# Kernel optimization log

Measured on AMD Instinct MI355X. Metric: run time of the kernel, lower is better.

Reference implementation:

```python
import jax, jax.numpy as jnp
import numpy as np

N = 100000  # nodes
E = 1600000  # directed edges

_DIMS = [("eg1", 3, 160), ("eg2", 160, 80), ("eg3", 80, 40), ("eg4", 40, 20),
         ("el1", 20, 10), ("el2", 10, 3), ("dl1", 3, 10), ("dl2", 10, 20),
         ("dg1", 20, 40), ("dg2", 40, 80), ("dg3", 80, 160), ("dg4", 160, 3)]


def _lin_init(key, ci, co):
    s = 1.0 / np.sqrt(ci)
    kw, kb = jax.random.split(key)
    w = jax.random.uniform(kw, (ci, co), jnp.float32, -s, s)
    b = jax.random.uniform(kb, (co,), jnp.float32, -s, s)
    return w, b


def setup_inputs():
    key = jax.random.key(0)
    k0, k1, k2 = jax.random.split(key, 3)
    x = jax.random.normal(k0, (N, 3), jnp.float32)
    src = jax.random.randint(k1, (E,), 0, N)
    dst = jax.random.randint(k2, (E,), 0, N)
    edge_index = jnp.stack([src, dst])  # [2, E] int32 indices
    out = {"x": x, "edge_index": edge_index}
    for i, (name, ci, co) in enumerate(_DIMS):
        w, b = _lin_init(jax.random.fold_in(key, i + 10), ci, co)
        out[name + "_w"] = w
        out[name + "_b"] = b
    return out


def _gcn(x, w, b, src, dst, norm):
    # PyG GCNConv: linear transform, then symmetric-normalized scatter-add.
    h = x @ w
    agg = jax.ops.segment_sum(h[src] * norm[:, None], dst, num_segments=N)
    return agg + b


def reference(x, edge_index, eg1_w, eg1_b, eg2_w, eg2_b, eg3_w, eg3_b, eg4_w, eg4_b,
              el1_w, el1_b, el2_w, el2_b, dl1_w, dl1_b, dl2_w, dl2_b,
              dg1_w, dg1_b, dg2_w, dg2_b, dg3_w, dg3_b, dg4_w, dg4_b):
    loops = jnp.arange(N)
    src = jnp.concatenate([edge_index[0], loops])  # add self-loops (PyG default)
    dst = jnp.concatenate([edge_index[1], loops])
    deg = jax.ops.segment_sum(jnp.ones(src.shape[0], x.dtype), dst, num_segments=N)
    dis = jnp.where(deg > 0, jax.lax.rsqrt(deg), 0.0)
    norm = dis[src] * dis[dst]  # D^-1/2 A D^-1/2 edge weights
    relu = jax.nn.relu
    h = relu(_gcn(x, eg1_w, eg1_b, src, dst, norm))
    h = relu(_gcn(h, eg2_w, eg2_b, src, dst, norm))
    h = relu(_gcn(h, eg3_w, eg3_b, src, dst, norm))
    h = relu(_gcn(h, eg4_w, eg4_b, src, dst, norm))
    h = relu(h @ el1_w + el1_b)
    h = h @ el2_w + el2_b  # latent [N, 3]
    h = relu(h @ dl1_w + dl1_b)
    h = relu(h @ dl2_w + dl2_b)
    h = relu(_gcn(h, dg1_w, dg1_b, src, dst, norm))
    h = relu(_gcn(h, dg2_w, dg2_b, src, dst, norm))
    h = relu(_gcn(h, dg3_w, dg3_b, src, dst, norm))
    h = jnp.tanh(_gcn(h, dg4_w, dg4_b, src, dst, norm))
    return h
```

## Files before the change

kernel.cpp:

```cpp
#include <hip/hip_runtime.h>
#include <hip/hip_fp16.h>
#include <math.h>

#define BS 256
static constexpr int NN = 100000;
static constexpr int EE = 1600000;
static constexpr int BUCKET_SH = 7;
static constexpr int NBUCKET = (NN + 127) >> BUCKET_SH;
static constexpr int NB_PART = 256;
static constexpr int CHUNK = EE / NB_PART;
static constexpr int NP_ = NBUCKET * NB_PART;
static constexpr int SCAN_ELEMS = 1024;
static constexpr int NPB = (NP_ + SCAN_ELEMS - 1) / SCAN_ELEMS;

static inline int cdiv(long long a, int b) { return (int)((a + b - 1) / b); }

typedef _Float16 half8 __attribute__((ext_vector_type(8)));
typedef float f32x4 __attribute__((ext_vector_type(4)));

template <int ACT>
__device__ __forceinline__ float act_f(float v) {
    if (ACT == 1) return fmaxf(v, 0.0f);
    if (ACT == 2) return tanhf(v);
    return v;
}

__device__ __forceinline__ unsigned short h16(float v) {
    return __half_as_ushort(__float2half(v));
}
__device__ __forceinline__ unsigned pack2h(float a, float b) {
    return (unsigned)h16(a) | ((unsigned)h16(b) << 16);
}
__device__ __forceinline__ float4 cvt4h(uint2 r) {
    float2 fa = __half22float2(*(const __half2*)&r.x);
    float2 fb = __half22float2(*(const __half2*)&r.y);
    return make_float4(fa.x, fa.y, fb.x, fb.y);
}
__device__ __forceinline__ void acc8h(uint4 r, float4& a, float4& b) {
    float2 f0 = __half22float2(*(const __half2*)&r.x);
    float2 f1 = __half22float2(*(const __half2*)&r.y);
    float2 f2 = __half22float2(*(const __half2*)&r.z);
    float2 f3 = __half22float2(*(const __half2*)&r.w);
    a.x += f0.x; a.y += f0.y; a.z += f1.x; a.w += f1.y;
    b.x += f2.x; b.y += f2.y; b.z += f3.x; b.w += f3.y;
}

template <int OUTM>
__device__ __forceinline__ void store1(float* out, size_t idx, float v, float dn) {
    if (OUTM == 0) out[idx] = v;
    else if (OUTM == 1) out[idx] = v * dn;
    else if (OUTM == 2) ((unsigned short*)out)[idx] = h16(v * dn);
    else ((unsigned short*)out)[idx] = h16(v);
}

__global__ __launch_bounds__(256) void k_hist(const int* __restrict__ dst,
                                              int* __restrict__ part_cnt) {
    __shared__ int h[NBUCKET];
    int b = blockIdx.x;
    for (int j = threadIdx.x; j < NBUCKET; j += 256) h[j] = 0;
    __syncthreads();
    int e0 = b * CHUNK;
    for (int k = threadIdx.x; k < CHUNK; k += 256)
        atomicAdd(&h[dst[e0 + k] >> BUCKET_SH], 1);
    __syncthreads();
    for (int j = threadIdx.x; j < NBUCKET; j += 256)
        part_cnt[j * NB_PART + b] = h[j];
}

__global__ void k_scanA(const int* __restrict__ in, int* __restrict__ outp,
                        int* __restrict__ bsums) {
    __shared__ int lds[BS];
    int base = blockIdx.x * SCAN_ELEMS;
    int t = threadIdx.x;
    int v[4];
    int s = 0;
#pragma unroll
    for (int j = 0; j < 4; ++j) {
        int idx = base + t * 4 + j;
        v[j] = (idx < NP_) ? in[idx] : 0;
        s += v[j];
    }
    lds[t] = s;
    __syncthreads();
    for (int off = 1; off < BS; off <<= 1) {
        int add = (t >= off) ? lds[t - off] : 0;
        __syncthreads();
        lds[t] += add;
        __syncthreads();
    }
    int run = lds[t] - s;
    if (t == BS - 1) bsums[blockIdx.x] = lds[BS - 1];
#pragma unroll
    for (int j = 0; j < 4; ++j) {
        int idx = base + t * 4 + j;
        if (idx < NP_) outp[idx] = run;
        run += v[j];
    }
}

__global__ void k_scanB(int* __restrict__ bsums) {
    if (threadIdx.x == 0 && blockIdx.x == 0) {
        int acc = 0;
        for (int i = 0; i < NPB; ++i) {
            int t = bsums[i];
            bsums[i] = acc;
            acc += t;
        }
    }
}

__global__ void k_scanC(int* __restrict__ outp, const int* __restrict__ bsums,
                        int* __restrict__ bbase) {
    int i = blockIdx.x * BS + threadIdx.x;
    if (i < NP_) {
        int v = outp[i] + bsums[i / SCAN_ELEMS];
        outp[i] = v;
        if ((i & (NB_PART - 1)) == 0) bbase[i / NB_PART] = v;
    }
    if (i == 0) bbase[NBUCKET] = EE;
}

__global__ __launch_bounds__(256) void k_part(const int* __restrict__ src,
                                              const int* __restrict__ dst,
                                              const int* __restrict__ scan_out,
                                              unsigned* __restrict__ epb) {
    __shared__ int cur[NBUCKET];
    int b = blockIdx.x;
    for (int j = threadIdx.x; j < NBUCKET; j += 256) cur[j] = scan_out[j * NB_PART + b];
    __syncthreads();
    int e0 = b * CHUNK;
    for (int k = threadIdx.x; k < CHUNK; k += 256) {
        int e = e0 + k;
        int d = dst[e];
        int s = src[e];
        int pos = atomicAdd(&cur[d >> BUCKET_SH], 1);
        epb[pos] = ((unsigned)(d & ((1 << BUCKET_SH) - 1)) << 17) | (unsigned)s;
    }
}

__global__ __launch_bounds__(256) void k_fine2(const int* __restrict__ bbase,
                                               const unsigned* __restrict__ epb,
                                               int* __restrict__ eidx,
                                               int* __restrict__ rowptr,
                                               float* __restrict__ dis) {
    __shared__ int hcnt[1 << BUCKET_SH];
    __shared__ int hoff[1 << BUCKET_SH];
    int b = blockIdx.x;
    int n0 = b << BUCKET_SH;
    int nloc = min(1 << BUCKET_SH, NN - n0);
    int t = threadIdx.x;
    if (t < (1 << BUCKET_SH)) hcnt[t] = 0;
    __syncthreads();
    int es = bbase[b], ee = bbase[b + 1];
    for (int k = es + t; k < ee; k += 256) atomicAdd(&hcnt[epb[k] >> 17], 1);
    __syncthreads();
    if (t < (1 << BUCKET_SH)) hoff[t] = hcnt[t];
    __syncthreads();
    for (int off = 1; off < (1 << BUCKET_SH); off <<= 1) {
        int add = (t >= off && t < (1 << BUCKET_SH)) ? hoff[t - off] : 0;
        __syncthreads();
        if (t < (1 << BUCKET_SH)) hoff[t] += add;
        __syncthreads();
    }
    if (t < nloc) {
        int excl = hoff[t] - hcnt[t];
        rowptr[n0 + t] = es + excl;
        dis[n0 + t] = rsqrtf((float)(hcnt[t] + 1));
    }
    __syncthreads();
    if (t < (1 << BUCKET_SH)) hoff[t] = es + hoff[t] - hcnt[t];
    __syncthreads();
    for (int k = es + t; k < ee; k += 256) {
        unsigned p = epb[k];
        int pos = atomicAdd(&hoff[p >> 17], 1);
        eidx[pos] = (int)(p & 0x1FFFFu);
    }
    if (b == NBUCKET - 1 && t == 0) rowptr[NN] = EE;
}

template <int C, int ACT, bool HASB, bool OUTH>
__global__ void k_gatherw(const unsigned short* __restrict__ g, const int* __restrict__ rowptr,
                          const int* __restrict__ eidx, const float* __restrict__ dis,
                          const float* __restrict__ b, float* __restrict__ out) {
    static_assert(C % 8 == 0, "C%8");
    constexpr int V = C / 8;
    int t = blockIdx.x * BS + threadIdx.x;
    if (t >= NN * V) return;
    int n = t / V, v = t % V;
    const uint4* g4 = (const uint4*)g;
    float4 accA = make_float4(0.f, 0.f, 0.f, 0.f);
    float4 accB = make_float4(0.f, 0.f, 0.f, 0.f);
    acc8h(g4[(size_t)n * V + v], accA, accB);
    int rs = rowptr[n], re = rowptr[n + 1];
    int k = rs;
    for (; k + 4 <= re; k += 4) {
        int s0 = eidx[k + 0], s1 = eidx[k + 1], s2 = eidx[k + 2], s3 = eidx[k + 3];
        uint4 r0 = g4[(size_t)s0 * V + v];
        uint4 r1 = g4[(size_t)s1 * V + v];
        uint4 r2 = g4[(size_t)s2 * V + v];
        uint4 r3 = g4[(size_t)s3 * V + v];
        acc8h(r0, accA, accB);
        acc8h(r1, accA, accB);
        acc8h(r2, accA, accB);
        acc8h(r3, accA, accB);
    }
    for (; k < re; ++k) {
        acc8h(g4[(size_t)eidx[k] * V + v], accA, accB);
    }
    float dn = dis[n];
    accA.x *= dn; accA.y *= dn; accA.z *= dn; accA.w *= dn;
    accB.x *= dn; accB.y *= dn; accB.z *= dn; accB.w *= dn;
    if (HASB) {
        float4 b0 = ((const float4*)b)[v * 2 + 0];
        float4 b1 = ((const float4*)b)[v * 2 + 1];
        accA.x += b0.x; accA.y += b0.y; accA.z += b0.z; accA.w += b0.w;
        accB.x += b1.x; accB.y += b1.y; accB.z += b1.z; accB.w += b1.w;
    }
    accA.x = act_f<ACT>(accA.x); accA.y = act_f<ACT>(accA.y);
    accA.z = act_f<ACT>(accA.z); accA.w = act_f<ACT>(accA.w);
    accB.x = act_f<ACT>(accB.x); accB.y = act_f<ACT>(accB.y);
    accB.z = act_f<ACT>(accB.z); accB.w = act_f<ACT>(accB.w);
    if (OUTH) {
        uint4 u;
        u.x = pack2h(accA.x, accA.y);
        u.y = pack2h(accA.z, accA.w);
        u.z = pack2h(accB.x, accB.y);
        u.w = pack2h(accB.z, accB.w);
        ((uint4*)out)[(size_t)n * V + v] = u;
    } else {
        float4* op = (float4*)out + (size_t)n * (C / 4) + v * 2;
        op[0] = accA;
        op[1] = accB;
    }
}

template <int C, int ACT, bool HASB, bool OUTH>
__global__ void k_gatherh(const unsigned short* __restrict__ g, const int* __restrict__ rowptr,
                          const int* __restrict__ eidx, const float* __restrict__ dis,
                          const float* __restrict__ b, float* __restrict__ out) {
    static_assert(C % 4 == 0, "C%4");
    constexpr int V = C / 4;
    int t = blockIdx.x * BS + threadIdx.x;
    if (t >= NN * V) return;
    int n = t / V, v = t % V;
    const uint2* g2 = (const uint2*)g;
    float4 acc = cvt4h(g2[(size_t)n * V + v]);
    int rs = rowptr[n], re = rowptr[n + 1];
    int k = rs;
    for (; k + 4 <= re; k += 4) {
        int s0 = eidx[k + 0], s1 = eidx[k + 1], s2 = eidx[k + 2], s3 = eidx[k + 3];
        uint2 r0 = g2[(size_t)s0 * V + v];
        uint2 r1 = g2[(size_t)s1 * V + v];
        uint2 r2 = g2[(size_t)s2 * V + v];
        uint2 r3 = g2[(size_t)s3 * V + v];
        float4 h0 = cvt4h(r0), h1 = cvt4h(r1), h2 = cvt4h(r2), h3 = cvt4h(r3);
        acc.x += (h0.x + h1.x) + (h2.x + h3.x);
        acc.y += (h0.y + h1.y) + (h2.y + h3.y);
        acc.z += (h0.z + h1.z) + (h2.z + h3.z);
        acc.w += (h0.w + h1.w) + (h2.w + h3.w);
    }
    for (; k < re; ++k) {
        float4 hv = cvt4h(g2[(size_t)eidx[k] * V + v]);
        acc.x += hv.x; acc.y += hv.y; acc.z += hv.z; acc.w += hv.w;
    }
    float dn = dis[n];
    acc.x *= dn; acc.y *= dn; acc.z *= dn; acc.w *= dn;
    if (HASB) {
        float4 bb = ((const float4*)b)[v];
        acc.x += bb.x; acc.y += bb.y; acc.z += bb.z; acc.w += bb.w;
    }
    acc.x = act_f<ACT>(acc.x);
    acc.y = act_f<ACT>(acc.y);
    acc.z = act_f<ACT>(acc.z);
    acc.w = act_f<ACT>(acc.w);
    if (OUTH) {
        uint2 u;
        u.x = pack2h(acc.x, acc.y);
        u.y = pack2h(acc.z, acc.w);
        ((uint2*)out)[(size_t)n * V + v] = u;
    } else {
        ((float4*)out)[(size_t)n * V + v] = acc;
    }
}

template <int ACT, bool HASB>
__global__ void k_gather3d(const float* __restrict__ g, const int* __restrict__ rowptr,
                           const int* __restrict__ eidx, const float* __restrict__ dis,
                           const float* __restrict__ b, float* __restrict__ out) {
    int n = blockIdx.x * BS + threadIdx.x;
    if (n >= NN) return;
    const float* gp = g + (size_t)n * 3;
    float a0 = gp[0], a1 = gp[1], a2 = gp[2];
    int rs = rowptr[n], re = rowptr[n + 1];
    int k = rs;
    for (; k + 4 <= re; k += 4) {
        const float* q0 = g + (size_t)eidx[k + 0] * 3;
        const float* q1 = g + (size_t)eidx[k + 1] * 3;
        const float* q2 = g + (size_t)eidx[k + 2] * 3;
        const float* q3 = g + (size_t)eidx[k + 3] * 3;
        float b00 = q0[0], b01 = q0[1], b02 = q0[2];
        float b10 = q1[0], b11 = q1[1], b12 = q1[2];
        float b20 = q2[0], b21 = q2[1], b22 = q2[2];
        float b30 = q3[0], b31 = q3[1], b32 = q3[2];
        a0 += (b00 + b10) + (b20 + b30);
        a1 += (b01 + b11) + (b21 + b31);
        a2 += (b02 + b12) + (b22 + b32);
    }
    for (; k < re; ++k) {
        const float* gq = g + (size_t)eidx[k] * 3;
        a0 += gq[0]; a1 += gq[1]; a2 += gq[2];
    }
    float dn = dis[n];
    a0 *= dn; a1 *= dn; a2 *= dn;
    if (HASB) { a0 += b[0]; a1 += b[1]; a2 += b[2]; }
    float* op = out + (size_t)n * 3;
    op[0] = act_f<ACT>(a0);
    op[1] = act_f<ACT>(a1);
    op[2] = act_f<ACT>(a2);
}

__global__ void k_scale3(const float* __restrict__ x, const float* __restrict__ dis,
                         float* __restrict__ g) {
    int i = blockIdx.x * BS + threadIdx.x;
    if (i < NN * 3) g[i] = x[i] * dis[i / 3];
}

__global__ __launch_bounds__(256) void k_latent(const unsigned short* __restrict__ in20,
                                                const float* __restrict__ el1_w, const float* __restrict__ el1_b,
                                                const float* __restrict__ el2_w, const float* __restrict__ el2_b,
                                                const float* __restrict__ dl1_w, const float* __restrict__ dl1_b,
                                                const float* __restrict__ dl2_w, const float* __restrict__ dl2_b,
                                                const float* __restrict__ dis,
                                                unsigned short* __restrict__ G) {
    __shared__ float w1[200], b1[10], w2[30], b2[3], w3[30], b3[10], w4[200], b4[20];
    int t = threadIdx.x;
    if (t < 200) w1[t] = el1_w[t];
    if (t < 10) b1[t] = el1_b[t];
    if (t < 30) w2[t] = el2_w[t];
    if (t < 3) b2[t] = el2_b[t];
    if (t < 30) w3[t] = dl1_w[t];
    if (t < 10) b3[t] = dl1_b[t];
    if (t < 200) w4[t] = dl2_w[t];
    if (t < 20) b4[t] = dl2_b[t];
    __syncthreads();
    int n = blockIdx.x * 256 + t;
    if (n >= NN) return;
    float h0[20];
    const uint2* ip = (const uint2*)in20 + (size_t)n * 5;
#pragma unroll
    for (int v = 0; v < 5; ++v) {
        float4 f = cvt4h(ip[v]);
        h0[v * 4 + 0] = f.x; h0[v * 4 + 1] = f.y;
        h0[v * 4 + 2] = f.z; h0[v * 4 + 3] = f.w;
    }
    float a1[10];
#pragma unroll
    for (int j = 0; j < 10; ++j) {
        float s = b1[j];
#pragma unroll
        for (int i = 0; i < 20; ++i) s = fmaf(h0[i], w1[i * 10 + j], s);
        a1[j] = fmaxf(s, 0.0f);
    }
    float a2[3];
#pragma unroll
    for (int j = 0; j < 3; ++j) {
        float s = b2[j];
#pragma unroll
        for (int i = 0; i < 10; ++i) s = fmaf(a1[i], w2[i * 3 + j], s);
        a2[j] = s;
    }
    float a3[10];
#pragma unroll
    for (int j = 0; j < 10; ++j) {
        float s = b3[j];
#pragma unroll
        for (int i = 0; i < 3; ++i) s = fmaf(a2[i], w3[i * 10 + j], s);
        a3[j] = fmaxf(s, 0.0f);
    }
    float dn = dis[n];
    uint2* gp = (uint2*)G + (size_t)n * 5;
#pragma unroll
    for (int v = 0; v < 5; ++v) {
        float o[4];
#pragma unroll
        for (int q = 0; q < 4; ++q) {
            int j = v * 4 + q;
            float s = b4[j];
#pragma unroll
            for (int i = 0; i < 10; ++i) s = fmaf(a3[i], w4[i * 20 + j], s);
            o[q] = fmaxf(s, 0.0f) * dn;
        }
        uint2 u;
        u.x = pack2h(o[0], o[1]);
        u.y = pack2h(o[2], o[3]);
        gp[v] = u;
    }
}

template <int K, int N, int ACT, bool HASB, int OUTM>
__global__ __launch_bounds__(256) void k_mm_mfma(const unsigned short* __restrict__ x,
                                                 const float* __restrict__ w,
                                                 const float* __restrict__ bias,
                                                 unsigned short* __restrict__ out,
                                                 const float* __restrict__ dis) {
    constexpr int KP = (K + 31) & ~31;
    constexpr int NT = (N + 15) / 16;
    constexpr int NPAD = NT * 16;
    constexpr int KC = KP / 32;
    constexpr int SP = KP + 8;
    __shared__ _Float16 Al[64 * SP];
    __shared__ _Float16 Wl[(KP / 8) * NPAD * 8];
    const int tid = threadIdx.x;
    const int n0 = blockIdx.x * 64;

    {
        constexpr int K4 = KP / 4;
        const uint2* x2 = (const uint2*)x;
        for (int i = tid; i < 64 * K4; i += 256) {
            int r = i / K4, k4 = i % K4;
            uint2 v = make_uint2(0u, 0u);
            int row = n0 + r;
            if (row < NN && k4 * 4 < K) v = x2[(size_t)row * (K / 4) + k4];
            *(uint2*)&Al[r * SP + k4 * 4] = v;
        }
    }
    for (int i = tid; i < KP * NPAD; i += 256) {
        int k = i / NPAD, n = i % NPAD;
        float v = (k < K && n < N) ? w[k * N + n] : 0.0f;
        Wl[(k >> 3) * NPAD * 8 + n * 8 + (k & 7)] = (_Float16)v;
    }
    __syncthreads();

    const int wave = tid >> 6;
    const int lane = tid & 63;
    const int lm = lane & 15;
    const int quad = lane >> 4;

    f32x4 acc[NT];
#pragma unroll
    for (int t = 0; t < NT; ++t) acc[t] = (f32x4){0.f, 0.f, 0.f, 0.f};

    const int arow = wave * 16 + lm;
#pragma unroll
    for (int kc = 0; kc < KC; ++kc) {
        half8 a = *(const half8*)&Al[arow * SP + kc * 32 + quad * 8];
#pragma unroll
        for (int t = 0; t < NT; ++t) {
            half8 bf = *(const half8*)&Wl[(kc * 4 + quad) * NPAD * 8 + (t * 16 + lm) * 8];
            acc[t] = __builtin_amdgcn_mfma_f32_16x16x32_f16(a, bf, acc[t], 0, 0, 0);
        }
    }
#pragma unroll
    for (int t = 0; t < NT; ++t) {
        int col = t * 16 + lm;
        if (col < N) {
            float bb = HASB ? bias[col] : 0.0f;
#pragma unroll
            for (int r = 0; r < 4; ++r) {
                int row = n0 + wave * 16 + quad * 4 + r;
                if (row < NN) {
                    float v = act_f<ACT>(acc[t][r] + bb);
                    if (OUTM == 2) v *= dis[row];
                    out[(size_t)row * N + col] = h16(v);
                }
            }
        }
    }
}

template <int CIN, int COUT, int ACT, int OUTM>
__global__ void k_mm_rowbcast(const float* __restrict__ x, const float* __restrict__ w,
                              const float* __restrict__ b, float* __restrict__ out) {
    static_assert(COUT % 4 == 0, "c4");
    constexpr int COUT4 = COUT / 4;
    int i = blockIdx.x * BS + threadIdx.x;
    if (i >= NN * COUT4) return;
    int n = i / COUT4, c4 = i % COUT4;
    const float4* w4 = (const float4*)w;
    float4 acc = ((const float4*)b)[c4];
    const float* xr = x + (size_t)n * CIN;
#pragma unroll
    for (int ci = 0; ci < CIN; ++ci) {
        float xv = xr[ci];
        float4 wv = w4[ci * COUT4 + c4];
        acc.x = fmaf(xv, wv.x, acc.x);
        acc.y = fmaf(xv, wv.y, acc.y);
        acc.z = fmaf(xv, wv.z, acc.z);
        acc.w = fmaf(xv, wv.w, acc.w);
    }
    acc.x = act_f<ACT>(acc.x); acc.y = act_f<ACT>(acc.y);
    acc.z = act_f<ACT>(acc.z); acc.w = act_f<ACT>(acc.w);
    if (OUTM == 3) {
        uint2 u;
        u.x = pack2h(acc.x, acc.y);
        u.y = pack2h(acc.z, acc.w);
        ((uint2*)out)[(size_t)n * COUT4 + c4] = u;
    } else {
        ((float4*)out)[(size_t)n * COUT4 + c4] = acc;
    }
}

template <int CIN, int COUT, int ACT, bool HASB, int OUTM, bool INH>
__global__ void k_mm_vec4(const float* __restrict__ x, const float* __restrict__ w,
                          const float* __restrict__ b, float* __restrict__ out,
                          const float* __restrict__ dis) {
    static_assert(CIN % 4 == 0 && COUT % 4 == 0, "align");
    constexpr int TM = 8;
    constexpr int CIN4 = CIN / 4;
    constexpr int COUT4 = COUT / 4;
    constexpr int RG = NN / TM;
    int i = blockIdx.x * BS + threadIdx.x;
    if (i >= RG * COUT4) return;
    int c4 = i % COUT4;
    int n0 = (i / COUT4) * TM;
    const float4* x4 = (const float4*)x;
    const uint2* xh = (const uint2*)x;
    const float4* w4 = (const float4*)w;
    float4 acc[TM];
    float4 bb = HASB ? ((const float4*)b)[c4] : make_float4(0.f, 0.f, 0.f, 0.f);
#pragma unroll
    for (int r = 0; r < TM; ++r) acc[r] = bb;
    for (int k4 = 0; k4 < CIN4; ++k4) {
        float4 wv[4];
#pragma unroll
        for (int j = 0; j < 4; ++j) wv[j] = w4[(size_t)(4 * k4 + j) * COUT4 + c4];
#pragma unroll
        for (int r = 0; r < TM; ++r) {
            float4 xv;
            if (INH) xv = cvt4h(xh[(size_t)(n0 + r) * CIN4 + k4]);
            else xv = x4[(size_t)(n0 + r) * CIN4 + k4];
            acc[r].x = fmaf(xv.x, wv[0].x, fmaf(xv.y, wv[1].x, fmaf(xv.z, wv[2].x, fmaf(xv.w, wv[3].x, acc[r].x))));
            acc[r].y = fmaf(xv.x, wv[0].y, fmaf(xv.y, wv[1].y, fmaf(xv.z, wv[2].y, fmaf(xv.w, wv[3].y, acc[r].y))));
            acc[r].z = fmaf(xv.x, wv[0].z, fmaf(xv.y, wv[1].z, fmaf(xv.z, wv[2].z, fmaf(xv.w, wv[3].z, acc[r].z))));
            acc[r].w = fmaf(xv.x, wv[0].w, fmaf(xv.y, wv[1].w, fmaf(xv.z, wv[2].w, fmaf(xv.w, wv[3].w, acc[r].w))));
        }
    }
#pragma unroll
    for (int r = 0; r < TM; ++r) {
        float vx = act_f<ACT>(acc[r].x), vy = act_f<ACT>(acc[r].y);
        float vz = act_f<ACT>(acc[r].z), vw = act_f<ACT>(acc[r].w);
        size_t gi = (size_t)(n0 + r) * COUT4 + c4;
        if (OUTM == 2) {
            float dn = dis[n0 + r];
            uint2 u;
            u.x = pack2h(vx * dn, vy * dn);
            u.y = pack2h(vz * dn, vw * dn);
            ((uint2*)out)[gi] = u;
        } else if (OUTM == 1) {
            float dn = dis[n0 + r];
            ((float4*)out)[gi] = make_float4(vx * dn, vy * dn, vz * dn, vw * dn);
        } else {
            ((float4*)out)[gi] = make_float4(vx, vy, vz, vw);
        }
    }
}

template <int CIN, int COUT, int ACT, bool HASB, int OUTM, bool INH>
__global__ void k_mm_vec(const float* __restrict__ x, const float* __restrict__ w,
                         const float* __restrict__ b, float* __restrict__ out,
                         const float* __restrict__ dis) {
    static_assert(CIN % 4 == 0, "CIN%4");
    constexpr int TM = 8;
    constexpr int CIN4 = CIN / 4;
    constexpr int RG = NN / TM;
    int i = blockIdx.x * BS + threadIdx.x;
    if (i >= RG * COUT) return;
    int c = i % COUT;
    int n0 = (i / COUT) * TM;
    float acc[TM];
    float bb = HASB ? b[c] : 0.0f;
#pragma unroll
    for (int r = 0; r < TM; ++r) acc[r] = bb;
    const float4* x4 = (const float4*)x;
    const uint2* xh = (const uint2*)x;
    for (int k = 0; k < CIN4; ++k) {
        float w0 = w[(4 * k + 0) * COUT + c];
        float w1 = w[(4 * k + 1) * COUT + c];
        float w2 = w[(4 * k + 2) * COUT + c];
        float w3 = w[(4 * k + 3) * COUT + c];
#pragma unroll
        for (int r = 0; r < TM; ++r) {
            float4 xv;
            if (INH) xv = cvt4h(xh[(size_t)(n0 + r) * CIN4 + k]);
            else xv = x4[(size_t)(n0 + r) * CIN4 + k];
            acc[r] = fmaf(xv.x, w0, fmaf(xv.y, w1, fmaf(xv.z, w2, fmaf(xv.w, w3, acc[r]))));
        }
    }
#pragma unroll
    for (int r = 0; r < TM; ++r) {
        int row = n0 + r;
        float dn = (OUTM == 1 || OUTM == 2) ? dis[row] : 0.0f;
        store1<OUTM>(out, (size_t)row * COUT + c, act_f<ACT>(acc[r]), dn);
    }
}

extern "C" void kernel_launch(void* const* d_in, const int* in_sizes, int n_in,
                              void* d_out, int out_size, void* d_ws, size_t ws_size,
                              hipStream_t stream) {
    const float* x = (const float*)d_in[0];
    const int* ei = (const int*)d_in[1];
    const int* src = ei;
    const int* dst = ei + EE;
    const float* eg1_w = (const float*)d_in[2];  const float* eg1_b = (const float*)d_in[3];
    const float* eg2_w = (const float*)d_in[4];  const float* eg2_b = (const float*)d_in[5];
    const float* eg3_w = (const float*)d_in[6];  const float* eg3_b = (const float*)d_in[7];
    const float* eg4_w = (const float*)d_in[8];  const float* eg4_b = (const float*)d_in[9];
    const float* el1_w = (const float*)d_in[10]; const float* el1_b = (const float*)d_in[11];
    const float* el2_w = (const float*)d_in[12]; const float* el2_b = (const float*)d_in[13];
    const float* dl1_w = (const float*)d_in[14]; const float* dl1_b = (const float*)d_in[15];
    const float* dl2_w = (const float*)d_in[16]; const float* dl2_b = (const float*)d_in[17];
    const float* dg1_w = (const float*)d_in[18]; const float* dg1_b = (const float*)d_in[19];
    const float* dg2_w = (const float*)d_in[20]; const float* dg2_b = (const float*)d_in[21];
    const float* dg3_w = (const float*)d_in[22]; const float* dg3_b = (const float*)d_in[23];
    const float* dg4_w = (const float*)d_in[24]; const float* dg4_b = (const float*)d_in[25];
    float* out = (float*)d_out;

    char* ws = (char*)d_ws;
    size_t off = 0;
    auto alloc = [&](size_t bytes) {
        void* p = ws + off;
        off += (bytes + 15) & ~(size_t)15;
        return p;
    };
    int* part_cnt = (int*)alloc(sizeof(int) * NP_);
    int* scan_out = (int*)alloc(sizeof(int) * NP_);
    int* bsums    = (int*)alloc(sizeof(int) * NPB);
    int* bbase    = (int*)alloc(sizeof(int) * (NBUCKET + 1));
    int* rowptr   = (int*)alloc(sizeof(int) * (NN + 1));
    float* dis    = (float*)alloc(sizeof(float) * NN);
    int* eidx     = (int*)alloc(sizeof(int) * EE);
    unsigned* epb = (unsigned*)alloc(sizeof(unsigned) * EE);
    unsigned short* G = (unsigned short*)alloc(sizeof(unsigned short) * 80 * (size_t)NN);
    float* bufA = (float*)alloc(sizeof(float) * 160 * (size_t)NN);
    float* bufB = (float*)alloc(sizeof(float) * 160 * (size_t)NN);

    k_hist<<<NB_PART, 256, 0, stream>>>(dst, part_cnt);
    k_scanA<<<NPB, BS, 0, stream>>>(part_cnt, scan_out, bsums);
    k_scanB<<<1, 64, 0, stream>>>(bsums);
    k_scanC<<<cdiv(NP_, BS), BS, 0, stream>>>(scan_out, bsums, bbase);
    k_part<<<NB_PART, 256, 0, stream>>>(src, dst, scan_out, epb);
    k_fine2<<<NBUCKET, 256, 0, stream>>>(bbase, epb, eidx, rowptr, dis);

    k_scale3<<<cdiv(3LL * NN, BS), BS, 0, stream>>>(x, dis, bufB);
    k_gather3d<0, false><<<cdiv(NN, BS), BS, 0, stream>>>(bufB, rowptr, eidx, dis, nullptr, bufA);
    k_mm_rowbcast<3, 160, 1, 3><<<cdiv(NN * 40LL, BS), BS, 0, stream>>>(bufA, eg1_w, eg1_b, bufB);

    k_mm_mfma<160, 80, 0, false, 2><<<cdiv(NN, 64), 256, 0, stream>>>(
        (const unsigned short*)bufB, eg2_w, nullptr, G, dis);
    k_gatherw<80, 1, true, true><<<cdiv(NN * 10LL, BS), BS, 0, stream>>>(G, rowptr, eidx, dis, eg2_b, bufA);

    k_mm_mfma<80, 40, 0, false, 2><<<cdiv(NN, 64), 256, 0, stream>>>(
        (const unsigned short*)bufA, eg3_w, nullptr, G, dis);
    k_gatherw<40, 1, true, true><<<cdiv(NN * 5LL, BS), BS, 0, stream>>>(G, rowptr, eidx, dis, eg3_b, bufB);

    k_mm_vec4<40, 20, 0, false, 2, true><<<cdiv((NN / 8) * 5LL, BS), BS, 0, stream>>>(
        bufB, eg4_w, nullptr, (float*)G, dis);
    k_gatherh<20, 1, true, true><<<cdiv(NN * 5LL, BS), BS, 0, stream>>>(G, rowptr, eidx, dis, eg4_b, bufA);

    k_latent<<<cdiv(NN, 256), 256, 0, stream>>>((const unsigned short*)bufA,
        el1_w, el1_b, el2_w, el2_b, dl1_w, dl1_b, dl2_w, dl2_b, dis, G);

    k_gatherh<20, 0, false, true><<<cdiv(NN * 5LL, BS), BS, 0, stream>>>(G, rowptr, eidx, dis, nullptr, bufA);
    k_mm_vec4<20, 40, 1, true, 2, true><<<cdiv((NN / 8) * 10LL, BS), BS, 0, stream>>>(
        bufA, dg1_w, dg1_b, (float*)G, dis);

    k_gatherw<40, 0, false, true><<<cdiv(NN * 5LL, BS), BS, 0, stream>>>(G, rowptr, eidx, dis, nullptr, bufB);
    k_mm_mfma<40, 80, 1, true, 2><<<cdiv(NN, 64), 256, 0, stream>>>(
        (const unsigned short*)bufB, dg2_w, dg2_b, G, dis);

    k_gatherw<80, 0, false, true><<<cdiv(NN * 10LL, BS), BS, 0, stream>>>(G, rowptr, eidx, dis, nullptr, bufA);
    k_mm_mfma<80, 160, 1, true, 3><<<cdiv(NN, 64), 256, 0, stream>>>(
        (const unsigned short*)bufA, dg3_w, dg3_b, (unsigned short*)bufB, nullptr);

    k_mm_vec<160, 3, 0, false, 1, true><<<cdiv((NN / 8) * 3LL, BS), BS, 0, stream>>>(bufB, dg4_w, nullptr, bufA, dis);
    k_gather3d<2, true><<<cdiv(NN, BS), BS, 0, stream>>>(bufA, rowptr, eidx, dis, dg4_b, out);
}
```

Before: 593.3 us.

## Pre-pack fp16 MFMA weights once and load operands directly from global

Adds a small per-layer kernel that converts each MFMA layer's fp32 weights into the padded fp16 fragment layout once per call. The MFMA matmul now reads A rows and weight fragments straight from global memory instead of staging them in LDS, which removes the per-block weight conversion, the LDS fill and the __syncthreads. The epilogue is reordered to loop over rows, hoisting the bias and dis loads. The trade-off is four extra tiny launches and uncached-looking global loads of B fragments that rely on L1/L2 reuse across blocks.

```diff
diff --git a/kernel.cpp b/kernel.cpp
--- a/kernel.cpp
+++ b/kernel.cpp
@@ -397,71 +397,70 @@
     }
 }
 
-template <int K, int N, int ACT, bool HASB, int OUTM>
-__global__ __launch_bounds__(256) void k_mm_mfma(const unsigned short* __restrict__ x,
-                                                 const float* __restrict__ w,
-                                                 const float* __restrict__ bias,
-                                                 unsigned short* __restrict__ out,
-                                                 const float* __restrict__ dis) {
+template <int K, int N>
+__global__ void k_wprep(const float* __restrict__ w, _Float16* __restrict__ wh) {
     constexpr int KP = (K + 31) & ~31;
     constexpr int NT = (N + 15) / 16;
     constexpr int NPAD = NT * 16;
+    int i = blockIdx.x * 256 + threadIdx.x;
+    if (i >= KP * NPAD) return;
+    int k = i / NPAD, n = i % NPAD;
+    float v = (k < K && n < N) ? w[k * N + n] : 0.0f;
+    wh[((size_t)(k >> 3) * NPAD + n) * 8 + (k & 7)] = (_Float16)v;
+}
+
+template <int K, int N, int ACT, bool HASB, int OUTM>
+__global__ __launch_bounds__(256) void k_mfma(const unsigned short* __restrict__ x,
+                                              const _Float16* __restrict__ wh,
+                                              const float* __restrict__ bias,
+                                              unsigned short* __restrict__ out,
+                                              const float* __restrict__ dis) {
+    static_assert(K % 8 == 0, "K%8");
+    constexpr int KP = (K + 31) & ~31;
     constexpr int KC = KP / 32;
-    constexpr int SP = KP + 8;
-    __shared__ _Float16 Al[64 * SP];
-    __shared__ _Float16 Wl[(KP / 8) * NPAD * 8];
-    const int tid = threadIdx.x;
-    const int n0 = blockIdx.x * 64;
-
-    {
-        constexpr int K4 = KP / 4;
-        const uint2* x2 = (const uint2*)x;
-        for (int i = tid; i < 64 * K4; i += 256) {
-            int r = i / K4, k4 = i % K4;
-            uint2 v = make_uint2(0u, 0u);
-            int row = n0 + r;
-            if (row < NN && k4 * 4 < K) v = x2[(size_t)row * (K / 4) + k4];
-            *(uint2*)&Al[r * SP + k4 * 4] = v;
-        }
-    }
-    for (int i = tid; i < KP * NPAD; i += 256) {
-        int k = i / NPAD, n = i % NPAD;
-        float v = (k < K && n < N) ? w[k * N + n] : 0.0f;
-        Wl[(k >> 3) * NPAD * 8 + n * 8 + (k & 7)] = (_Float16)v;
-    }
-    __syncthreads();
-
-    const int wave = tid >> 6;
-    const int lane = tid & 63;
+    constexpr int NT = (N + 15) / 16;
+    constexpr int NPAD = NT * 16;
+    const int wid = blockIdx.x * 4 + (threadIdx.x >> 6);
+    const int lane = threadIdx.x & 63;
     const int lm = lane & 15;
     const int quad = lane >> 4;
+    const int arow = wid * 16 + lm;
 
     f32x4 acc[NT];
 #pragma unroll
     for (int t = 0; t < NT; ++t) acc[t] = (f32x4){0.f, 0.f, 0.f, 0.f};
 
-    const int arow = wave * 16 + lm;
+    const _Float16* xr = (const _Float16*)x + (size_t)arow * K;
 #pragma unroll
     for (int kc = 0; kc < KC; ++kc) {
-        half8 a = *(const half8*)&Al[arow * SP + kc * 32 + quad * 8];
+        int k0 = kc * 32 + quad * 8;
+        half8 a = (half8)(_Float16)0;
+        if (arow < NN && k0 < K) a = *(const half8*)(xr + k0);
 #pragma unroll
         for (int t = 0; t < NT; ++t) {
-            half8 bf = *(const half8*)&Wl[(kc * 4 + quad) * NPAD * 8 + (t * 16 + lm) * 8];
+            half8 bf = *(const half8*)&wh[((size_t)(kc * 4 + quad) * NPAD + t * 16 + lm) * 8];
             acc[t] = __builtin_amdgcn_mfma_f32_16x16x32_f16(a, bf, acc[t], 0, 0, 0);
         }
     }
+
+    float bb[NT];
 #pragma unroll
     for (int t = 0; t < NT; ++t) {
         int col = t * 16 + lm;
-        if (col < N) {
-            float bb = HASB ? bias[col] : 0.0f;
-#pragma unroll
-            for (int r = 0; r < 4; ++r) {
-                int row = n0 + wave * 16 + quad * 4 + r;
-                if (row < NN) {
-                    float v = act_f<ACT>(acc[t][r] + bb);
-                    if (OUTM == 2) v *= dis[row];
-                    out[(size_t)row * N + col] = h16(v);
+        bb[t] = (HASB && col < N) ? bias[col] : 0.0f;
+    }
+#pragma unroll
+    for (int r = 0; r < 4; ++r) {
+        int orow = wid * 16 + quad * 4 + r;
+        if (orow < NN) {
+            float dn = (OUTM == 2) ? dis[orow] : 1.0f;
+#pragma unroll
+            for (int t = 0; t < NT; ++t) {
+                int col = t * 16 + lm;
+                if (col < N) {
+                    float v = act_f<ACT>(acc[t][r] + bb[t]);
+                    if (OUTM == 2) v *= dn;
+                    out[(size_t)orow * N + col] = h16(v);
                 }
             }
         }
@@ -633,6 +632,10 @@
     unsigned short* G = (unsigned short*)alloc(sizeof(unsigned short) * 80 * (size_t)NN);
     float* bufA = (float*)alloc(sizeof(float) * 160 * (size_t)NN);
     float* bufB = (float*)alloc(sizeof(float) * 160 * (size_t)NN);
+    _Float16* whEg2 = (_Float16*)alloc(sizeof(_Float16) * (160 / 8) * 80 * 8);
+    _Float16* whEg3 = (_Float16*)alloc(sizeof(_Float16) * (96 / 8) * 48 * 8);
+    _Float16* whDg2 = (_Float16*)alloc(sizeof(_Float16) * (64 / 8) * 80 * 8);
+    _Float16* whDg3 = (_Float16*)alloc(sizeof(_Float16) * (96 / 8) * 160 * 8);
 
     k_hist<<<NB_PART, 256, 0, stream>>>(dst, part_cnt);
     k_scanA<<<NPB, BS, 0, stream>>>(part_cnt, scan_out, bsums);
@@ -641,16 +644,21 @@
     k_part<<<NB_PART, 256, 0, stream>>>(src, dst, scan_out, epb);
     k_fine2<<<NBUCKET, 256, 0, stream>>>(bbase, epb, eidx, rowptr, dis);
 
+    k_wprep<160, 80><<<cdiv(160 * 80, 256), 256, 0, stream>>>(eg2_w, whEg2);
+    k_wprep<80, 40><<<cdiv(96 * 48, 256), 256, 0, stream>>>(eg3_w, whEg3);
+    k_wprep<40, 80><<<cdiv(64 * 80, 256), 256, 0, stream>>>(dg2_w, whDg2);
+    k_wprep<80, 160><<<cdiv(96 * 160, 256), 256, 0, stream>>>(dg3_w, whDg3);
+
     k_scale3<<<cdiv(3LL * NN, BS), BS, 0, stream>>>(x, dis, bufB);
     k_gather3d<0, false><<<cdiv(NN, BS), BS, 0, stream>>>(bufB, rowptr, eidx, dis, nullptr, bufA);
     k_mm_rowbcast<3, 160, 1, 3><<<cdiv(NN * 40LL, BS), BS, 0, stream>>>(bufA, eg1_w, eg1_b, bufB);
 
-    k_mm_mfma<160, 80, 0, false, 2><<<cdiv(NN, 64), 256, 0, stream>>>(
-        (const unsigned short*)bufB, eg2_w, nullptr, G, dis);
+    k_mfma<160, 80, 0, false, 2><<<cdiv(NN, 64), 256, 0, stream>>>(
+        (const unsigned short*)bufB, whEg2, nullptr, G, dis);
     k_gatherw<80, 1, true, true><<<cdiv(NN * 10LL, BS), BS, 0, stream>>>(G, rowptr, eidx, dis, eg2_b, bufA);
 
-    k_mm_mfma<80, 40, 0, false, 2><<<cdiv(NN, 64), 256, 0, stream>>>(
-        (const unsigned short*)bufA, eg3_w, nullptr, G, dis);
+    k_mfma<80, 40, 0, false, 2><<<cdiv(NN, 64), 256, 0, stream>>>(
+        (const unsigned short*)bufA, whEg3, nullptr, G, dis);
     k_gatherw<40, 1, true, true><<<cdiv(NN * 5LL, BS), BS, 0, stream>>>(G, rowptr, eidx, dis, eg3_b, bufB);
 
     k_mm_vec4<40, 20, 0, false, 2, true><<<cdiv((NN / 8) * 5LL, BS), BS, 0, stream>>>(
@@ -665,12 +673,12 @@
         bufA, dg1_w, dg1_b, (float*)G, dis);
 
     k_gatherw<40, 0, false, true><<<cdiv(NN * 5LL, BS), BS, 0, stream>>>(G, rowptr, eidx, dis, nullptr, bufB);
-    k_mm_mfma<40, 80, 1, true, 2><<<cdiv(NN, 64), 256, 0, stream>>>(
-        (const unsigned short*)bufB, dg2_w, dg2_b, G, dis);
+    k_mfma<40, 80, 1, true, 2><<<cdiv(NN, 64), 256, 0, stream>>>(
+        (const unsigned short*)bufB, whDg2, dg2_b, G, dis);
 
     k_gatherw<80, 0, false, true><<<cdiv(NN * 10LL, BS), BS, 0, stream>>>(G, rowptr, eidx, dis, nullptr, bufA);
-    k_mm_mfma<80, 160, 1, true, 3><<<cdiv(NN, 64), 256, 0, stream>>>(
-        (const unsigned short*)bufA, dg3_w, dg3_b, (unsigned short*)bufB, nullptr);
+    k_mfma<80, 160, 1, true, 3><<<cdiv(NN, 64), 256, 0, stream>>>(
+        (const unsigned short*)bufA, whDg3, dg3_b, (unsigned short*)bufB, nullptr);
 
     k_mm_vec<160, 3, 0, false, 1, true><<<cdiv((NN / 8) * 3LL, BS), BS, 0, stream>>>(bufB, dg4_w, nullptr, bufA, dis);
     k_gather3d<2, true><<<cdiv(NN, BS), BS, 0, stream>>>(bufA, rowptr, eidx, dis, dg4_b, out);
```

New measurement: 527.4 us. -11.1%, faster.
